# Performance work log

Measured on AMD Instinct MI355X. Metric: run time of the kernel, lower is better.

Reference implementation:

```python
import jax, jax.numpy as jnp
import numpy as np

N, E, B = 50000, 800000, 64
IN, H, OUT = 64, 128, 64


def _gcn_norm(edge_index, num_nodes):
    # PyG gcn_norm with add_self_loops=True: A_hat = A + I, norm = d^-1/2[src]*d^-1/2[dst]
    loop = jnp.arange(num_nodes)
    src = jnp.concatenate([edge_index[0], loop])
    dst = jnp.concatenate([edge_index[1], loop])
    deg = jax.ops.segment_sum(jnp.ones_like(dst, dtype=jnp.float32), dst,
                              num_segments=num_nodes)  # >= 1 due to self-loops
    dis = deg ** -0.5
    norm = dis[src] * dis[dst]  # [E+N]
    return src, dst, norm


def _gcn_layer(x, W, b, src, dst, norm, num_nodes):
    h = x @ W                                   # linear first (GCNConv order)
    msg = h[src] * norm[:, None]                # gather + normalize, [E+N, H]
    out = jax.ops.segment_sum(msg, dst, num_segments=num_nodes)  # scatter-add
    return out + b


def setup_inputs() -> dict:
    key = jax.random.key(0)
    ks = jax.random.split(key, 12)
    x = jax.random.normal(ks[0], (N, IN), dtype=jnp.float32)
    edge_index = jax.random.randint(ks[1], (2, E), 0, N, dtype=jnp.int64)
    batch = jnp.sort(jax.random.randint(ks[2], (N,), 0, B, dtype=jnp.int64))

    def lin(k, fan_in, fan_out):
        s = 1.0 / np.sqrt(fan_in)
        return jax.random.uniform(k, (fan_in, fan_out), jnp.float32, -s, s)

    return {
        "x": x, "edge_index": edge_index, "batch": batch,
        "W1": lin(ks[3], IN, H), "b1": jnp.zeros((H,), jnp.float32),
        "W2": lin(ks[4], H, H),  "b2": jnp.zeros((H,), jnp.float32),
        "W3": lin(ks[5], H, H),  "b3": jnp.zeros((H,), jnp.float32),
        "W4": lin(ks[6], H, OUT), "b4": jnp.zeros((OUT,), jnp.float32),
    }


def reference(x, edge_index, batch, W1, b1, W2, b2, W3, b3, W4, b4):
    src, dst, norm = _gcn_norm(edge_index, N)
    h = jax.nn.relu(_gcn_layer(x, W1, b1, src, dst, norm, N))
    h = jax.nn.relu(_gcn_layer(h, W2, b2, src, dst, norm, N))
    # global mean pool over graphs
    sums = jax.ops.segment_sum(h, batch, num_segments=B)          # [B, H]
    cnts = jax.ops.segment_sum(jnp.ones((N,), jnp.float32), batch, num_segments=B)
    pooled = sums / jnp.maximum(cnts, 1.0)[:, None]
    # MLP head
    return jax.nn.relu(pooled @ W3 + b3) @ W4 + b4                # [B, OUT]
```

## Files before the change

kernel.cpp:

```cpp
#include <hip/hip_runtime.h>


__device__ __forceinline__ float ldf(const void* p, long long i, int f32) {
    if (f32) return ((const float*)p)[i];
    unsigned int u = ((const unsigned short*)p)[i];
    return __uint_as_float(u << 16);
}
__device__ __forceinline__ float bfl(unsigned int u) { return __uint_as_float(u << 16); }
__device__ __forceinline__ float bfh(unsigned int u) { return __uint_as_float(u & 0xFFFF0000u); }
__device__ __forceinline__ int ld_idx(const int* p, long long i, int i64) {
    return i64 ? p[2 * i] : p[i];
}
__device__ __forceinline__ unsigned short f2bf(float v) {
    unsigned int x = __float_as_uint(v);
    return (unsigned short)((x + 0x7FFFu + ((x >> 16) & 1u)) >> 16);
}
__device__ __forceinline__ int clampi(int v, int lo, int hi) {
    return v < lo ? lo : (v > hi ? hi : v);
}

#define OW1 0
#define OB1 8192
#define OW2 8320
#define OB2 24704
// ... 69 lines not shown
        if (j < m) rank[base + j] = r[j];
}

__global__ void gnn_scan1(const int* __restrict__ cnt, int* __restrict__ excl,
                          int* __restrict__ sums, float* __restrict__ dis, int N) {
    __shared__ int sh[256];
    int t = threadIdx.x;
    int i = blockIdx.x * 256 + t;
    int v = (i < N) ? cnt[i] : 0;
    sh[t] = v;
    __syncthreads();
    for (int off = 1; off < 256; off <<= 1) {
        int a = (t >= off) ? sh[t - off] : 0;
        __syncthreads();
        sh[t] += a;
        __syncthreads();
    }
    if (i < N) {
        excl[i] = sh[t] - v;
        dis[i] = rsqrtf((float)v + 1.0f);
    }
    if (t == 255) sums[blockIdx.x] = sh[255];
}

__global__ void gnn_scan2(int* __restrict__ sums, int nb) {
    __shared__ int sh[256];
    int t = threadIdx.x;
    int v = (t < nb) ? sums[t] : 0;
    sh[t] = v;
    __syncthreads();
    for (int off = 1; off < 256; off <<= 1) {
        int a = (t >= off) ? sh[t - off] : 0;
        __syncthreads();
        sh[t] += a;
        __syncthreads();
    }
    if (t < nb) sums[t] = sh[t] - v;
}

template <bool SMALLN>
__global__ void gnn_fill(const int* __restrict__ ei, const int* __restrict__ excl,
                         const int* __restrict__ bsums, const int* __restrict__ rank,
                         void* __restrict__ csr, int E, int N,
                         const int* __restrict__ flags,
                         const void* __restrict__ x, const float* __restrict__ dis,
                         unsigned short* __restrict__ xb) {
    const int tid = blockIdx.x * 256 + threadIdx.x;
    const int i64 = flags[1];
    if (tid < E) {
        int s = clampi(ld_idx(ei, (long long)tid, i64), 0, N - 1);
        int d = clampi(ld_idx(ei, (long long)E + tid, i64), 0, N - 1);
        int pos = excl[d] + bsums[d >> 8] + rank[tid];
        if (SMALLN) ((unsigned short*)csr)[pos] = (unsigned short)s;
        else        ((int*)csr)[pos] = s;
    }
    const int f32 = flags[0];
    const int total = N * 16;
    const int stride = gridDim.x * 256;
    for (int j = tid; j < total; j += stride) {
        int n = j >> 4;
        float dn = dis[n];
        float v0, v1, v2, v3;
        if (f32) {
            float4 xv = ((const float4*)x)[j];
            v0 = xv.x; v1 = xv.y; v2 = xv.z; v3 = xv.w;
        } else {
            ushort4 xv = ((const ushort4*)x)[j];
            v0 = bfl(xv.x); v1 = bfl(xv.y); v2 = bfl(xv.z); v3 = bfl(xv.w);
        }
        ushort4 o;
        o.x = f2bf(v0 * dn); o.y = f2bf(v1 * dn);
        o.z = f2bf(v2 * dn); o.w = f2bf(v3 * dn);
        ((ushort4*)xb)[j] = o;
    }
}

template <bool SMALLN>
__device__ __forceinline__ int csr_at(const void* csr, int e) {
    return SMALLN ? (int)((const unsigned short*)csr)[e] : ((const int*)csr)[e];
}


template <bool SMALLN>
__global__ __launch_bounds__(128) void gnn_aggx_lin1(const unsigned short* __restrict__ xb,
                                                     const int* __restrict__ excl,
                                                     const int* __restrict__ bsums,
                                                     const void* __restrict__ csr,
                                                     const float* __restrict__ dis,
                                                     const float* __restrict__ Wf,
                                                     const float* __restrict__ bias,
                                                     int N, int E, float* __restrict__ out) {
    __shared__ float Xs[16 * 64];
    const int t = threadIdx.x;
    const int nbase = blockIdx.x * 16;
    const int wave = t >> 6;
    const int lane = t & 63;
    const int eslot = lane >> 3;
    const int fg = lane & 7;

    for (int pass = 0; pass < 8; ++pass) {
        const int ln = pass * 2 + wave;
        const int n = nbase + ln;
        float a0 = 0.f, a1 = 0.f, a2 = 0.f, a3 = 0.f;
        float a4 = 0.f, a5 = 0.f, a6 = 0.f, a7 = 0.f;
        if (n < N) {
            int beg = excl[n] + bsums[n >> 8];
            int end = (n + 1 < N) ? (excl[n + 1] + bsums[(n + 1) >> 8]) : E;
            for (int e = beg + eslot; e < end; e += 8) {
                int s = csr_at<SMALLN>(csr, e);
                uint4 u = *(const uint4*)(xb + (long long)s * 64 + fg * 8);
                a0 += bfl(u.x); a1 += bfh(u.x);
                a2 += bfl(u.y); a3 += bfh(u.y);
                a4 += bfl(u.z); a5 += bfh(u.z);
                a6 += bfl(u.w); a7 += bfh(u.w);
            }
        }
#pragma unroll
        for (int m = 8; m <= 32; m <<= 1) {
            a0 += __shfl_xor(a0, m); a1 += __shfl_xor(a1, m);
            a2 += __shfl_xor(a2, m); a3 += __shfl_xor(a3, m);
            a4 += __shfl_xor(a4, m); a5 += __shfl_xor(a5, m);
            a6 += __shfl_xor(a6, m); a7 += __shfl_xor(a7, m);
        }
        if (n < N && eslot == 0) {
            float dn = dis[n];
            uint4 u = *(const uint4*)(xb + (long long)n * 64 + fg * 8);
            float4 o0, o1;
            o0.x = (a0 + bfl(u.x)) * dn; o0.y = (a1 + bfh(u.x)) * dn;
            o0.z = (a2 + bfl(u.y)) * dn; o0.w = (a3 + bfh(u.y)) * dn;
            o1.x = (a4 + bfl(u.z)) * dn; o1.y = (a5 + bfh(u.z)) * dn;
            o1.z = (a6 + bfl(u.w)) * dn; o1.w = (a7 + bfh(u.w)) * dn;
            *(float4*)&Xs[ln * 64 + fg * 8]     = o0;
            *(float4*)&Xs[ln * 64 + fg * 8 + 4] = o1;
        }
    }
    __syncthreads();

    const int fgB = t & 31, ng = t >> 5;
    const int f0 = fgB * 4, n0 = ng * 4;
    const float4* Xs4 = (const float4*)Xs;
    const float4* Wp  = (const float4*)Wf;
    float4 acc[4];
#pragma unroll
    for (int j = 0; j < 4; ++j) acc[j] = make_float4(0.f, 0.f, 0.f, 0.f);
#pragma unroll 4
    for (int k4 = 0; k4 < 16; ++k4) {
        const float4 wa = Wp[(4 * k4 + 0) * 32 + fgB];
        const float4 wb = Wp[(4 * k4 + 1) * 32 + fgB];
        const float4 wc = Wp[(4 * k4 + 2) * 32 + fgB];
        const float4 wd = Wp[(4 * k4 + 3) * 32 + fgB];
#pragma unroll
        for (int j = 0; j < 4; ++j) {
            const float4 xv = Xs4[(n0 + j) * 16 + k4];
            acc[j].x = fmaf(xv.x, wa.x, acc[j].x); acc[j].y = fmaf(xv.x, wa.y, acc[j].y);
            acc[j].z = fmaf(xv.x, wa.z, acc[j].z); acc[j].w = fmaf(xv.x, wa.w, acc[j].w);
            acc[j].x = fmaf(xv.y, wb.x, acc[j].x); acc[j].y = fmaf(xv.y, wb.y, acc[j].y);
            acc[j].z = fmaf(xv.y, wb.z, acc[j].z); acc[j].w = fmaf(xv.y, wb.w, acc[j].w);
            acc[j].x = fmaf(xv.z, wc.x, acc[j].x); acc[j].y = fmaf(xv.z, wc.y, acc[j].y);
            acc[j].z = fmaf(xv.z, wc.z, acc[j].z); acc[j].w = fmaf(xv.z, wc.w, acc[j].w);
            acc[j].x = fmaf(xv.w, wd.x, acc[j].x); acc[j].y = fmaf(xv.w, wd.y, acc[j].y);
            acc[j].z = fmaf(xv.w, wd.z, acc[j].z); acc[j].w = fmaf(xv.w, wd.w, acc[j].w);
        }
    }
    const float4 b = *(const float4*)&bias[f0];
#pragma unroll
    for (int j = 0; j < 4; ++j) {
        int n = nbase + n0 + j;
        if (n >= N) continue;
        float4 a = acc[j];
        a.x = fmaxf(a.x + b.x, 0.f);
        a.y = fmaxf(a.y + b.y, 0.f);
        a.z = fmaxf(a.z + b.z, 0.f);
        a.w = fmaxf(a.w + b.w, 0.f);
        *(float4*)(out + (long long)n * 128 + f0) = a;
    }
}


template <int K, bool RELU, bool OUTBF>
__global__ __launch_bounds__(128) void gnn_linear(const float* __restrict__ X,
                                                  const float* __restrict__ Wf,
                                                  const float* __restrict__ bias,
                                                  const float* __restrict__ dis,
                                                  int N, void* __restrict__ out) {
    __shared__ float Xs[16 * K];
    const int t = threadIdx.x;
    const int nbase = blockIdx.x * 16;

#pragma unroll
    for (int it = 0; it < K / 32; ++it) {
        int i4 = t + it * 128;
        int n = nbase + (i4 * 4) / K;
        float4 v = make_float4(0.f, 0.f, 0.f, 0.f);
        if (n < N) v = ((const float4*)X)[(long long)nbase * (K / 4) + i4];
        ((float4*)Xs)[i4] = v;
    }
    __syncthreads();

    const int fg = t & 31, ng = t >> 5;
    const int f0 = fg * 4, n0 = ng * 4;
    const float4* Xs4 = (const float4*)Xs;
    const float4* Wp  = (const float4*)Wf;
    float4 acc[4];
#pragma unroll
    for (int j = 0; j < 4; ++j) acc[j] = make_float4(0.f, 0.f, 0.f, 0.f);
#pragma unroll 4
    for (int k4 = 0; k4 < K / 4; ++k4) {
        const float4 wa = Wp[(4 * k4 + 0) * 32 + fg];
        const float4 wb = Wp[(4 * k4 + 1) * 32 + fg];
        const float4 wc = Wp[(4 * k4 + 2) * 32 + fg];
        const float4 wd = Wp[(4 * k4 + 3) * 32 + fg];
#pragma unroll
        for (int j = 0; j < 4; ++j) {
            const float4 xv = Xs4[(n0 + j) * (K / 4) + k4];
            acc[j].x = fmaf(xv.x, wa.x, acc[j].x); acc[j].y = fmaf(xv.x, wa.y, acc[j].y);
            acc[j].z = fmaf(xv.x, wa.z, acc[j].z); acc[j].w = fmaf(xv.x, wa.w, acc[j].w);
            acc[j].x = fmaf(xv.y, wb.x, acc[j].x); acc[j].y = fmaf(xv.y, wb.y, acc[j].y);
            acc[j].z = fmaf(xv.y, wb.z, acc[j].z); acc[j].w = fmaf(xv.y, wb.w, acc[j].w);
            acc[j].x = fmaf(xv.z, wc.x, acc[j].x); acc[j].y = fmaf(xv.z, wc.y, acc[j].y);
            acc[j].z = fmaf(xv.z, wc.z, acc[j].z); acc[j].w = fmaf(xv.z, wc.w, acc[j].w);
            acc[j].x = fmaf(xv.w, wd.x, acc[j].x); acc[j].y = fmaf(xv.w, wd.y, acc[j].y);
            acc[j].z = fmaf(xv.w, wd.z, acc[j].z); acc[j].w = fmaf(xv.w, wd.w, acc[j].w);
        }
    }
#pragma unroll
    for (int j = 0; j < 4; ++j) {
        int n = nbase + n0 + j;
        if (n >= N) continue;
        float4 a = acc[j];
        if (RELU) {
            const float4 b = *(const float4*)&bias[f0];
            a.x = fmaxf(a.x + b.x, 0.f);
            a.y = fmaxf(a.y + b.y, 0.f);
            a.z = fmaxf(a.z + b.z, 0.f);
            a.w = fmaxf(a.w + b.w, 0.f);
        }
        if (OUTBF) {
            const float dn = dis[n];
            a.x *= dn; a.y *= dn; a.z *= dn; a.w *= dn;
            uint2 u;
            u.x = (unsigned int)f2bf(a.x) | ((unsigned int)f2bf(a.y) << 16);
            u.y = (unsigned int)f2bf(a.z) | ((unsigned int)f2bf(a.w) << 16);
            *(uint2*)((unsigned short*)out + (long long)n * 128 + f0) = u;
        } else {
            *(float4*)((float*)out + (long long)n * 128 + f0) = a;
        }
    }
}


template <bool SMALLN>
__global__ __launch_bounds__(256) void gnn_agg_bf(const unsigned short* __restrict__ A2,
                                                  const int* __restrict__ excl,
                                                  const int* __restrict__ bsums,
                                                  const void* __restrict__ csr,
                                                  const float* __restrict__ dis,
                                                  const float* __restrict__ bias,
                                                  float* __restrict__ outC, int N, int E) {
    const int t = threadIdx.x;
    const int lane = t & 63;
    const int n = blockIdx.x * 4 + (t >> 6);
    if (n >= N) return;
    const int eslot = lane >> 4;
    const int fg = lane & 15;
    float a0 = 0.f, a1 = 0.f, a2 = 0.f, a3 = 0.f;
    float a4 = 0.f, a5 = 0.f, a6 = 0.f, a7 = 0.f;
    int beg = excl[n] + bsums[n >> 8];
    int end = (n + 1 < N) ? (excl[n + 1] + bsums[(n + 1) >> 8]) : E;
    for (int e = beg + eslot; e < end; e += 4) {
        int s = csr_at<SMALLN>(csr, e);
        uint4 u = *(const uint4*)(A2 + (long long)s * 128 + fg * 8);
        a0 += bfl(u.x); a1 += bfh(u.x);
        a2 += bfl(u.y); a3 += bfh(u.y);
        a4 += bfl(u.z); a5 += bfh(u.z);
        a6 += bfl(u.w); a7 += bfh(u.w);
    }
#pragma unroll
    for (int m = 16; m <= 32; m <<= 1) {
        a0 += __shfl_xor(a0, m); a1 += __shfl_xor(a1, m);
        a2 += __shfl_xor(a2, m); a3 += __shfl_xor(a3, m);
        a4 += __shfl_xor(a4, m); a5 += __shfl_xor(a5, m);
        a6 += __shfl_xor(a6, m); a7 += __shfl_xor(a7, m);
    }
    if (lane < 16) {
        float dn = dis[n];
        uint4 u = *(const uint4*)(A2 + (long long)n * 128 + fg * 8);
        const float4 bA = *(const float4*)&bias[fg * 8];
        const float4 bB = *(const float4*)&bias[fg * 8 + 4];
        float4 o0, o1;
        o0.x = fmaxf((a0 + bfl(u.x)) * dn + bA.x, 0.f);
        o0.y = fmaxf((a1 + bfh(u.x)) * dn + bA.y, 0.f);
        o0.z = fmaxf((a2 + bfl(u.y)) * dn + bA.z, 0.f);
        o0.w = fmaxf((a3 + bfh(u.y)) * dn + bA.w, 0.f);
        o1.x = fmaxf((a4 + bfl(u.z)) * dn + bB.x, 0.f);
        o1.y = fmaxf((a5 + bfh(u.z)) * dn + bB.y, 0.f);
        o1.z = fmaxf((a6 + bfl(u.w)) * dn + bB.z, 0.f);
        o1.w = fmaxf((a7 + bfh(u.w)) * dn + bB.w, 0.f);
        *(float4*)(outC + (long long)n * 128 + fg * 8)     = o0;
        *(float4*)(outC + (long long)n * 128 + fg * 8 + 4) = o1;
    }
}


#define PSTRIP 32
__global__ __launch_bounds__(128) void gnn_pool(const float* __restrict__ h,
                                                const int* __restrict__ batch,
                                                const int* __restrict__ flags,
                                                float* __restrict__ pooled, int N, int B) {
    int i64 = flags[1];
    int f = threadIdx.x;
    int n0 = blockIdx.x * PSTRIP;
    if (n0 >= N) return;
    int nend = min(n0 + PSTRIP, N);
    int cur = clampi(ld_idx(batch, n0, i64), 0, B - 1);
    float acc = 0.0f;
    for (int n = n0; n < nend; ++n) {
        int b = clampi(ld_idx(batch, n, i64), 0, B - 1);
        if (b != cur) {
            atomicAdd(&pooled[cur * 128 + f], acc);
            acc = 0.0f; cur = b;
        }
        acc += h[(long long)n * 128 + f];
    }
    atomicAdd(&pooled[cur * 128 + f], acc);
}


__global__ __launch_bounds__(128) void gnn_head(const float* __restrict__ pooled,
                                                const int* __restrict__ batch,
                                                const float* __restrict__ W3,
                                                const float* __restrict__ b3,
                                                const float* __restrict__ W4,
                                                const float* __restrict__ b4,
                                                const int* __restrict__ flags,
                                                void* __restrict__ outv, int N) {
    __shared__ float xs[128];
    __shared__ float rs[128];
    __shared__ float cinv;
    int b = blockIdx.x, f = threadIdx.x;
    if (f == 0) {
        int i64 = flags[1];
        int L = 0, R = N;
        while (L < R) { int m = (L + R) >> 1; if (ld_idx(batch, m, i64) < b) L = m + 1; else R = m; }
        int lo = L;
        L = 0; R = N;
        while (L < R) { int m = (L + R) >> 1; if (ld_idx(batch, m, i64) < b + 1) L = m + 1; else R = m; }
        cinv = 1.0f / fmaxf((float)(L - lo), 1.0f);
    }
    __syncthreads();
    xs[f] = pooled[b * 128 + f] * cinv;
    __syncthreads();
    float acc = b3[f];
    for (int k = 0; k < 128; ++k) acc = fmaf(xs[k], W3[k * 128 + f], acc);
    rs[f] = fmaxf(acc, 0.f);
    __syncthreads();
    if (f < 64) {
        float a2 = b4[f];
        for (int k = 0; k < 128; ++k) a2 = fmaf(rs[k], W4[k * 64 + f], a2);
        if (flags[0]) ((float*)outv)[b * 64 + f] = a2;
        else          ((unsigned short*)outv)[b * 64 + f] = f2bf(a2);
    }
}


extern "C" void kernel_launch(void* const* d_in, const int* in_sizes, int n_in,
                              void* d_out, int out_size, void* d_ws, size_t ws_size,
                              hipStream_t stream) {
    const void* x  = d_in[0];
    const int* ei  = (const int*)d_in[1];
    const int* bat = (const int*)d_in[2];

    const int N = in_sizes[0] / 64;
    const int E = in_sizes[1] / 2;
    const int B = out_size / 64;
    const bool smalln = (N < 65536);

    char* p = (char*)d_ws;
    auto alloc = [&](size_t bytes) { void* q = (void*)p; p += (bytes + 255) & ~(size_t)255; return q; };
    int*   flags    = (int*)alloc(256);
    float* wsW      = (float*)alloc((size_t)OTOT * 4);
    int*   degcnt   = (int*)alloc((size_t)N * 4);
    float* dis      = (float*)alloc((size_t)N * 4);
    int*   excl     = (int*)alloc((size_t)N * 4);
    int*   bsums    = (int*)alloc(1024);
    int*   rank     = (int*)alloc((size_t)E * 4);
    void*  csr      = alloc((size_t)E * (smalln ? 2 : 4));
    unsigned short* xb = (unsigned short*)alloc((size_t)N * 64 * 2);
    float* H1       = (float*)alloc((size_t)N * 128 * 4);
    float* C2       = (float*)alloc((size_t)N * 128 * 4);
    unsigned short* A2 = (unsigned short*)alloc((size_t)N * 128 * 2);
    float* pooled   = (float*)alloc((size_t)B * 128 * 4);
    (void)ws_size; (void)n_in;

    const int nbN = (N + 255) / 256;

    gnn_prep<<<512, 256, 0, stream>>>(d_in[3], d_in[4], d_in[5], d_in[6],
                                      d_in[7], d_in[8], d_in[9], d_in[10],
                                      ei, flags, degcnt, pooled, wsW, N, B);

    gnn_hist<<<(E + 1023) / 1024, 256, 0, stream>>>(ei, E, N, flags, degcnt, rank);
    gnn_scan1<<<nbN, 256, 0, stream>>>(degcnt, excl, bsums, dis, N);
    gnn_scan2<<<1, 256, 0, stream>>>(bsums, nbN);
    if (smalln)
        gnn_fill<true><<<(E + 255) / 256, 256, 0, stream>>>(ei, excl, bsums, rank, csr, E, N,
                                                            flags, x, dis, xb);
    else
        gnn_fill<false><<<(E + 255) / 256, 256, 0, stream>>>(ei, excl, bsums, rank, csr, E, N,
                                                             flags, x, dis, xb);

    const int nlin = (N + 15) / 16;
    const int nagg = (N + 3) / 4;

    if (smalln)
        gnn_aggx_lin1<true><<<nlin, 128, 0, stream>>>(xb, excl, bsums, csr, dis,
                                                      wsW + OW1, wsW + OB1, N, E, H1);
    else
        gnn_aggx_lin1<false><<<nlin, 128, 0, stream>>>(xb, excl, bsums, csr, dis,
                                                       wsW + OW1, wsW + OB1, N, E, H1);

    gnn_linear<128, false, true><<<nlin, 128, 0, stream>>>(H1, wsW + OW2, wsW + OB2, dis, N, (void*)A2);
    if (smalln)
        gnn_agg_bf<true><<<nagg, 256, 0, stream>>>(A2, excl, bsums, csr, dis, wsW + OB2, C2, N, E);
    else
        gnn_agg_bf<false><<<nagg, 256, 0, stream>>>(A2, excl, bsums, csr, dis, wsW + OB2, C2, N, E);

    gnn_pool<<<(N + PSTRIP - 1) / PSTRIP, 128, 0, stream>>>(C2, bat, flags, pooled, N, B);
    gnn_head<<<B, 128, 0, stream>>>(pooled, bat, wsW + OW3, wsW + OB3,
                                    wsW + OW4, wsW + OB4, flags, d_out, N);
}
```

Measured before the change: 278.6 us.

## Fuse layer-1 aggregation, lin1 and lin2; remap aggregation to one node per lane group

Merges the layer-1 aggregate+linear kernel with the following 128x128 linear, so H1 stays in shared memory and its fp32 round trip through global memory plus one launch go away. Both aggregation kernels now give each lane group a whole node with a 4-way unrolled edge loop, replacing the edge-split layout and its cross-lane shuffle reduction, and the Xs tile row stride is padded to avoid bank conflicts. The cost is that each lane group processes a whole node serially, so load balance now depends on the degree variance within a wave.

Result: faster. 261.7 us (-6.1%).

```diff
diff --git a/kernel.cpp b/kernel.cpp
--- a/kernel.cpp
+++ b/kernel.cpp
@@ -175,168 +175,140 @@
 
 
 template <bool SMALLN>
-__global__ __launch_bounds__(128) void gnn_aggx_lin1(const unsigned short* __restrict__ xb,
-                                                     const int* __restrict__ excl,
-                                                     const int* __restrict__ bsums,
-                                                     const void* __restrict__ csr,
-                                                     const float* __restrict__ dis,
-                                                     const float* __restrict__ Wf,
-                                                     const float* __restrict__ bias,
-                                                     int N, int E, float* __restrict__ out) {
-    __shared__ float Xs[16 * 64];
+__global__ __launch_bounds__(128) void gnn_l1l2(const unsigned short* __restrict__ xb,
+                                                const int* __restrict__ excl,
+                                                const int* __restrict__ bsums,
+                                                const void* __restrict__ csr,
+                                                const float* __restrict__ dis,
+                                                const float* __restrict__ W1,
+                                                const float* __restrict__ b1,
+                                                const float* __restrict__ W2,
+                                                int N, int E,
+                                                unsigned short* __restrict__ A2) {
+    __shared__ float Xs[16 * 68];
+    __shared__ float Hs[16 * 128];
     const int t = threadIdx.x;
     const int nbase = blockIdx.x * 16;
-    const int wave = t >> 6;
     const int lane = t & 63;
-    const int eslot = lane >> 3;
+    const int nd = (t >> 6) * 8 + (lane >> 3);
     const int fg = lane & 7;
-
-    for (int pass = 0; pass < 8; ++pass) {
-        const int ln = pass * 2 + wave;
-        const int n = nbase + ln;
-        float a0 = 0.f, a1 = 0.f, a2 = 0.f, a3 = 0.f;
-        float a4 = 0.f, a5 = 0.f, a6 = 0.f, a7 = 0.f;
-        if (n < N) {
-            int beg = excl[n] + bsums[n >> 8];
-            int end = (n + 1 < N) ? (excl[n + 1] + bsums[(n + 1) >> 8]) : E;
-            for (int e = beg + eslot; e < end; e += 8) {
-                int s = csr_at<SMALLN>(csr, e);
-                uint4 u = *(const uint4*)(xb + (long long)s * 64 + fg * 8);
-                a0 += bfl(u.x); a1 += bfh(u.x);
-                a2 += bfl(u.y); a3 += bfh(u.y);
-                a4 += bfl(u.z); a5 += bfh(u.z);
-                a6 += bfl(u.w); a7 += bfh(u.w);
-            }
-        }
-#pragma unroll
-        for (int m = 8; m <= 32; m <<= 1) {
-            a0 += __shfl_xor(a0, m); a1 += __shfl_xor(a1, m);
-            a2 += __shfl_xor(a2, m); a3 += __shfl_xor(a3, m);
-            a4 += __shfl_xor(a4, m); a5 += __shfl_xor(a5, m);
-            a6 += __shfl_xor(a6, m); a7 += __shfl_xor(a7, m);
-        }
-        if (n < N && eslot == 0) {
-            float dn = dis[n];
-            uint4 u = *(const uint4*)(xb + (long long)n * 64 + fg * 8);
-            float4 o0, o1;
-            o0.x = (a0 + bfl(u.x)) * dn; o0.y = (a1 + bfh(u.x)) * dn;
-            o0.z = (a2 + bfl(u.y)) * dn; o0.w = (a3 + bfh(u.y)) * dn;
-            o1.x = (a4 + bfl(u.z)) * dn; o1.y = (a5 + bfh(u.z)) * dn;
-            o1.z = (a6 + bfl(u.w)) * dn; o1.w = (a7 + bfh(u.w)) * dn;
-            *(float4*)&Xs[ln * 64 + fg * 8]     = o0;
-            *(float4*)&Xs[ln * 64 + fg * 8 + 4] = o1;
-        }
+    const int n = nbase + nd;
+
+    if (n < N) {
+        const float dn = dis[n];
+        uint4 us = *(const uint4*)(xb + (long long)n * 64 + fg * 8);
+        float a0 = bfl(us.x), a1 = bfh(us.x), a2 = bfl(us.y), a3 = bfh(us.y);
+        float a4 = bfl(us.z), a5 = bfh(us.z), a6 = bfl(us.w), a7 = bfh(us.w);
+        int beg = excl[n] + bsums[n >> 8];
+        int end = (n + 1 < N) ? (excl[n + 1] + bsums[(n + 1) >> 8]) : E;
+        int e = beg;
+        for (; e + 4 <= end; e += 4) {
+            int s0 = csr_at<SMALLN>(csr, e),     s1 = csr_at<SMALLN>(csr, e + 1);
+            int s2 = csr_at<SMALLN>(csr, e + 2), s3 = csr_at<SMALLN>(csr, e + 3);
+            uint4 u0 = *(const uint4*)(xb + (long long)s0 * 64 + fg * 8);
+            uint4 u1 = *(const uint4*)(xb + (long long)s1 * 64 + fg * 8);
+            uint4 u2 = *(const uint4*)(xb + (long long)s2 * 64 + fg * 8);
+            uint4 u3 = *(const uint4*)(xb + (long long)s3 * 64 + fg * 8);
+            a0 += bfl(u0.x); a1 += bfh(u0.x); a2 += bfl(u0.y); a3 += bfh(u0.y);
+            a4 += bfl(u0.z); a5 += bfh(u0.z); a6 += bfl(u0.w); a7 += bfh(u0.w);
+            a0 += bfl(u1.x); a1 += bfh(u1.x); a2 += bfl(u1.y); a3 += bfh(u1.y);
+            a4 += bfl(u1.z); a5 += bfh(u1.z); a6 += bfl(u1.w); a7 += bfh(u1.w);
+            a0 += bfl(u2.x); a1 += bfh(u2.x); a2 += bfl(u2.y); a3 += bfh(u2.y);
+            a4 += bfl(u2.z); a5 += bfh(u2.z); a6 += bfl(u2.w); a7 += bfh(u2.w);
+            a0 += bfl(u3.x); a1 += bfh(u3.x); a2 += bfl(u3.y); a3 += bfh(u3.y);
+            a4 += bfl(u3.z); a5 += bfh(u3.z); a6 += bfl(u3.w); a7 += bfh(u3.w);
+        }
+        for (; e < end; ++e) {
+            int s = csr_at<SMALLN>(csr, e);
+            uint4 u = *(const uint4*)(xb + (long long)s * 64 + fg * 8);
+            a0 += bfl(u.x); a1 += bfh(u.x); a2 += bfl(u.y); a3 += bfh(u.y);
+            a4 += bfl(u.z); a5 += bfh(u.z); a6 += bfl(u.w); a7 += bfh(u.w);
+        }
+        float4 o0, o1;
+        o0.x = a0 * dn; o0.y = a1 * dn; o0.z = a2 * dn; o0.w = a3 * dn;
+        o1.x = a4 * dn; o1.y = a5 * dn; o1.z = a6 * dn; o1.w = a7 * dn;
+        *(float4*)&Xs[nd * 68 + fg * 8]     = o0;
+        *(float4*)&Xs[nd * 68 + fg * 8 + 4] = o1;
+    } else {
+        float4 z = make_float4(0.f, 0.f, 0.f, 0.f);
+        *(float4*)&Xs[nd * 68 + fg * 8]     = z;
+        *(float4*)&Xs[nd * 68 + fg * 8 + 4] = z;
     }
     __syncthreads();
 
     const int fgB = t & 31, ng = t >> 5;
     const int f0 = fgB * 4, n0 = ng * 4;
-    const float4* Xs4 = (const float4*)Xs;
-    const float4* Wp  = (const float4*)Wf;
-    float4 acc[4];
-#pragma unroll
-    for (int j = 0; j < 4; ++j) acc[j] = make_float4(0.f, 0.f, 0.f, 0.f);
+    {
+        const float4* Wp = (const float4*)W1;
+        float4 acc[4];
+#pragma unroll
+        for (int j = 0; j < 4; ++j) acc[j] = make_float4(0.f, 0.f, 0.f, 0.f);
 #pragma unroll 4
-    for (int k4 = 0; k4 < 16; ++k4) {
-        const float4 wa = Wp[(4 * k4 + 0) * 32 + fgB];
-        const float4 wb = Wp[(4 * k4 + 1) * 32 + fgB];
-        const float4 wc = Wp[(4 * k4 + 2) * 32 + fgB];
-        const float4 wd = Wp[(4 * k4 + 3) * 32 + fgB];
+        for (int k4 = 0; k4 < 16; ++k4) {
+            const float4 wa = Wp[(4 * k4 + 0) * 32 + fgB];
+            const float4 wb = Wp[(4 * k4 + 1) * 32 + fgB];
+            const float4 wc = Wp[(4 * k4 + 2) * 32 + fgB];
+            const float4 wd = Wp[(4 * k4 + 3) * 32 + fgB];
+#pragma unroll
+            for (int j = 0; j < 4; ++j) {
+                const float4 xv = *(const float4*)&Xs[(n0 + j) * 68 + k4 * 4];
+                acc[j].x = fmaf(xv.x, wa.x, acc[j].x); acc[j].y = fmaf(xv.x, wa.y, acc[j].y);
+                acc[j].z = fmaf(xv.x, wa.z, acc[j].z); acc[j].w = fmaf(xv.x, wa.w, acc[j].w);
+                acc[j].x = fmaf(xv.y, wb.x, acc[j].x); acc[j].y = fmaf(xv.y, wb.y, acc[j].y);
+                acc[j].z = fmaf(xv.y, wb.z, acc[j].z); acc[j].w = fmaf(xv.y, wb.w, acc[j].w);
+                acc[j].x = fmaf(xv.z, wc.x, acc[j].x); acc[j].y = fmaf(xv.z, wc.y, acc[j].y);
+                acc[j].z = fmaf(xv.z, wc.z, acc[j].z); acc[j].w = fmaf(xv.z, wc.w, acc[j].w);
+                acc[j].x = fmaf(xv.w, wd.x, acc[j].x); acc[j].y = fmaf(xv.w, wd.y, acc[j].y);
+                acc[j].z = fmaf(xv.w, wd.z, acc[j].z); acc[j].w = fmaf(xv.w, wd.w, acc[j].w);
+            }
+        }
+        const float4 b = *(const float4*)&b1[f0];
 #pragma unroll
         for (int j = 0; j < 4; ++j) {
-            const float4 xv = Xs4[(n0 + j) * 16 + k4];
-            acc[j].x = fmaf(xv.x, wa.x, acc[j].x); acc[j].y = fmaf(xv.x, wa.y, acc[j].y);
-            acc[j].z = fmaf(xv.x, wa.z, acc[j].z); acc[j].w = fmaf(xv.x, wa.w, acc[j].w);
-            acc[j].x = fmaf(xv.y, wb.x, acc[j].x); acc[j].y = fmaf(xv.y, wb.y, acc[j].y);
-            acc[j].z = fmaf(xv.y, wb.z, acc[j].z); acc[j].w = fmaf(xv.y, wb.w, acc[j].w);
-            acc[j].x = fmaf(xv.z, wc.x, acc[j].x); acc[j].y = fmaf(xv.z, wc.y, acc[j].y);
-            acc[j].z = fmaf(xv.z, wc.z, acc[j].z); acc[j].w = fmaf(xv.z, wc.w, acc[j].w);
-            acc[j].x = fmaf(xv.w, wd.x, acc[j].x); acc[j].y = fmaf(xv.w, wd.y, acc[j].y);
-            acc[j].z = fmaf(xv.w, wd.z, acc[j].z); acc[j].w = fmaf(xv.w, wd.w, acc[j].w);
-        }
-    }
-    const float4 b = *(const float4*)&bias[f0];
-#pragma unroll
-    for (int j = 0; j < 4; ++j) {
-        int n = nbase + n0 + j;
-        if (n >= N) continue;
-        float4 a = acc[j];
-        a.x = fmaxf(a.x + b.x, 0.f);
-        a.y = fmaxf(a.y + b.y, 0.f);
-        a.z = fmaxf(a.z + b.z, 0.f);
-        a.w = fmaxf(a.w + b.w, 0.f);
-        *(float4*)(out + (long long)n * 128 + f0) = a;
-    }
-}
-
-
-template <int K, bool RELU, bool OUTBF>
-__global__ __launch_bounds__(128) void gnn_linear(const float* __restrict__ X,
-                                                  const float* __restrict__ Wf,
-                                                  const float* __restrict__ bias,
-                                                  const float* __restrict__ dis,
-                                                  int N, void* __restrict__ out) {
-    __shared__ float Xs[16 * K];
-    const int t = threadIdx.x;
-    const int nbase = blockIdx.x * 16;
-
-#pragma unroll
-    for (int it = 0; it < K / 32; ++it) {
-        int i4 = t + it * 128;
-        int n = nbase + (i4 * 4) / K;
-        float4 v = make_float4(0.f, 0.f, 0.f, 0.f);
-        if (n < N) v = ((const float4*)X)[(long long)nbase * (K / 4) + i4];
-        ((float4*)Xs)[i4] = v;
-    }
-    __syncthreads();
-
-    const int fg = t & 31, ng = t >> 5;
-    const int f0 = fg * 4, n0 = ng * 4;
-    const float4* Xs4 = (const float4*)Xs;
-    const float4* Wp  = (const float4*)Wf;
-    float4 acc[4];
-#pragma unroll
-    for (int j = 0; j < 4; ++j) acc[j] = make_float4(0.f, 0.f, 0.f, 0.f);
-#pragma unroll 4
-    for (int k4 = 0; k4 < K / 4; ++k4) {
-        const float4 wa = Wp[(4 * k4 + 0) * 32 + fg];
-        const float4 wb = Wp[(4 * k4 + 1) * 32 + fg];
-        const float4 wc = Wp[(4 * k4 + 2) * 32 + fg];
-        const float4 wd = Wp[(4 * k4 + 3) * 32 + fg];
-#pragma unroll
-        for (int j = 0; j < 4; ++j) {
-            const float4 xv = Xs4[(n0 + j) * (K / 4) + k4];
-            acc[j].x = fmaf(xv.x, wa.x, acc[j].x); acc[j].y = fmaf(xv.x, wa.y, acc[j].y);
-            acc[j].z = fmaf(xv.x, wa.z, acc[j].z); acc[j].w = fmaf(xv.x, wa.w, acc[j].w);
-            acc[j].x = fmaf(xv.y, wb.x, acc[j].x); acc[j].y = fmaf(xv.y, wb.y, acc[j].y);
-            acc[j].z = fmaf(xv.y, wb.z, acc[j].z); acc[j].w = fmaf(xv.y, wb.w, acc[j].w);
-            acc[j].x = fmaf(xv.z, wc.x, acc[j].x); acc[j].y = fmaf(xv.z, wc.y, acc[j].y);
-            acc[j].z = fmaf(xv.z, wc.z, acc[j].z); acc[j].w = fmaf(xv.z, wc.w, acc[j].w);
-            acc[j].x = fmaf(xv.w, wd.x, acc[j].x); acc[j].y = fmaf(xv.w, wd.y, acc[j].y);
-            acc[j].z = fmaf(xv.w, wd.z, acc[j].z); acc[j].w = fmaf(xv.w, wd.w, acc[j].w);
-        }
-    }
-#pragma unroll
-    for (int j = 0; j < 4; ++j) {
-        int n = nbase + n0 + j;
-        if (n >= N) continue;
-        float4 a = acc[j];
-        if (RELU) {
-            const float4 b = *(const float4*)&bias[f0];
+            float4 a = acc[j];
             a.x = fmaxf(a.x + b.x, 0.f);
             a.y = fmaxf(a.y + b.y, 0.f);
             a.z = fmaxf(a.z + b.z, 0.f);
             a.w = fmaxf(a.w + b.w, 0.f);
-        }
-        if (OUTBF) {
-            const float dn = dis[n];
+            *(float4*)&Hs[(n0 + j) * 128 + f0] = a;
+        }
+    }
+    __syncthreads();
+    {
+        const float4* Wp = (const float4*)W2;
+        float4 acc[4];
+#pragma unroll
+        for (int j = 0; j < 4; ++j) acc[j] = make_float4(0.f, 0.f, 0.f, 0.f);
+#pragma unroll 4
+        for (int k4 = 0; k4 < 32; ++k4) {
+            const float4 wa = Wp[(4 * k4 + 0) * 32 + fgB];
+            const float4 wb = Wp[(4 * k4 + 1) * 32 + fgB];
+            const float4 wc = Wp[(4 * k4 + 2) * 32 + fgB];
+            const float4 wd = Wp[(4 * k4 + 3) * 32 + fgB];
+#pragma unroll
+            for (int j = 0; j < 4; ++j) {
+                const float4 xv = *(const float4*)&Hs[(n0 + j) * 128 + k4 * 4];
+                acc[j].x = fmaf(xv.x, wa.x, acc[j].x); acc[j].y = fmaf(xv.x, wa.y, acc[j].y);
+                acc[j].z = fmaf(xv.x, wa.z, acc[j].z); acc[j].w = fmaf(xv.x, wa.w, acc[j].w);
+                acc[j].x = fmaf(xv.y, wb.x, acc[j].x); acc[j].y = fmaf(xv.y, wb.y, acc[j].y);
+                acc[j].z = fmaf(xv.y, wb.z, acc[j].z); acc[j].w = fmaf(xv.y, wb.w, acc[j].w);
+                acc[j].x = fmaf(xv.z, wc.x, acc[j].x); acc[j].y = fmaf(xv.z, wc.y, acc[j].y);
+                acc[j].z = fmaf(xv.z, wc.z, acc[j].z); acc[j].w = fmaf(xv.z, wc.w, acc[j].w);
+                acc[j].x = fmaf(xv.w, wd.x, acc[j].x); acc[j].y = fmaf(xv.w, wd.y, acc[j].y);
+                acc[j].z = fmaf(xv.w, wd.z, acc[j].z); acc[j].w = fmaf(xv.w, wd.w, acc[j].w);
+            }
+        }
+#pragma unroll
+        for (int j = 0; j < 4; ++j) {
+            int nn = nbase + n0 + j;
+            if (nn >= N) continue;
+            const float dn = dis[nn];
+            float4 a = acc[j];
             a.x *= dn; a.y *= dn; a.z *= dn; a.w *= dn;
             uint2 u;
             u.x = (unsigned int)f2bf(a.x) | ((unsigned int)f2bf(a.y) << 16);
             u.y = (unsigned int)f2bf(a.z) | ((unsigned int)f2bf(a.w) << 16);
-            *(uint2*)((unsigned short*)out + (long long)n * 128 + f0) = u;
-        } else {
-            *(float4*)((float*)out + (long long)n * 128 + f0) = a;
+            *(uint2*)(A2 + (long long)nn * 128 + f0) = u;
         }
     }
 }
@@ -352,46 +324,51 @@
                                                   float* __restrict__ outC, int N, int E) {
     const int t = threadIdx.x;
     const int lane = t & 63;
-    const int n = blockIdx.x * 4 + (t >> 6);
+    const int n = blockIdx.x * 16 + (t >> 6) * 4 + (lane >> 4);
     if (n >= N) return;
-    const int eslot = lane >> 4;
     const int fg = lane & 15;
-    float a0 = 0.f, a1 = 0.f, a2 = 0.f, a3 = 0.f;
-    float a4 = 0.f, a5 = 0.f, a6 = 0.f, a7 = 0.f;
+    const float dn = dis[n];
+    uint4 us = *(const uint4*)(A2 + (long long)n * 128 + fg * 8);
+    float a0 = bfl(us.x), a1 = bfh(us.x), a2 = bfl(us.y), a3 = bfh(us.y);
+    float a4 = bfl(us.z), a5 = bfh(us.z), a6 = bfl(us.w), a7 = bfh(us.w);
     int beg = excl[n] + bsums[n >> 8];
     int end = (n + 1 < N) ? (excl[n + 1] + bsums[(n + 1) >> 8]) : E;
-    for (int e = beg + eslot; e < end; e += 4) {
+    int e = beg;
+    for (; e + 4 <= end; e += 4) {
+        int s0 = csr_at<SMALLN>(csr, e),     s1 = csr_at<SMALLN>(csr, e + 1);
+        int s2 = csr_at<SMALLN>(csr, e + 2), s3 = csr_at<SMALLN>(csr, e + 3);
+        uint4 u0 = *(const uint4*)(A2 + (long long)s0 * 128 + fg * 8);
+        uint4 u1 = *(const uint4*)(A2 + (long long)s1 * 128 + fg * 8);
+        uint4 u2 = *(const uint4*)(A2 + (long long)s2 * 128 + fg * 8);
+        uint4 u3 = *(const uint4*)(A2 + (long long)s3 * 128 + fg * 8);
+        a0 += bfl(u0.x); a1 += bfh(u0.x); a2 += bfl(u0.y); a3 += bfh(u0.y);
+        a4 += bfl(u0.z); a5 += bfh(u0.z); a6 += bfl(u0.w); a7 += bfh(u0.w);
+        a0 += bfl(u1.x); a1 += bfh(u1.x); a2 += bfl(u1.y); a3 += bfh(u1.y);
+        a4 += bfl(u1.z); a5 += bfh(u1.z); a6 += bfl(u1.w); a7 += bfh(u1.w);
+        a0 += bfl(u2.x); a1 += bfh(u2.x); a2 += bfl(u2.y); a3 += bfh(u2.y);
+        a4 += bfl(u2.z); a5 += bfh(u2.z); a6 += bfl(u2.w); a7 += bfh(u2.w);
+        a0 += bfl(u3.x); a1 += bfh(u3.x); a2 += bfl(u3.y); a3 += bfh(u3.y);
+        a4 += bfl(u3.z); a5 += bfh(u3.z); a6 += bfl(u3.w); a7 += bfh(u3.w);
+    }
+    for (; e < end; ++e) {
         int s = csr_at<SMALLN>(csr, e);
         uint4 u = *(const uint4*)(A2 + (long long)s * 128 + fg * 8);
-        a0 += bfl(u.x); a1 += bfh(u.x);
-        a2 += bfl(u.y); a3 += bfh(u.y);
-        a4 += bfl(u.z); a5 += bfh(u.z);
-        a6 += bfl(u.w); a7 += bfh(u.w);
-    }
-#pragma unroll
-    for (int m = 16; m <= 32; m <<= 1) {
-        a0 += __shfl_xor(a0, m); a1 += __shfl_xor(a1, m);
-        a2 += __shfl_xor(a2, m); a3 += __shfl_xor(a3, m);
-        a4 += __shfl_xor(a4, m); a5 += __shfl_xor(a5, m);
-        a6 += __shfl_xor(a6, m); a7 += __shfl_xor(a7, m);
-    }
-    if (lane < 16) {
-        float dn = dis[n];
-        uint4 u = *(const uint4*)(A2 + (long long)n * 128 + fg * 8);
-        const float4 bA = *(const float4*)&bias[fg * 8];
-        const float4 bB = *(const float4*)&bias[fg * 8 + 4];
-        float4 o0, o1;
-        o0.x = fmaxf((a0 + bfl(u.x)) * dn + bA.x, 0.f);
-        o0.y = fmaxf((a1 + bfh(u.x)) * dn + bA.y, 0.f);
-        o0.z = fmaxf((a2 + bfl(u.y)) * dn + bA.z, 0.f);
-        o0.w = fmaxf((a3 + bfh(u.y)) * dn + bA.w, 0.f);
-        o1.x = fmaxf((a4 + bfl(u.z)) * dn + bB.x, 0.f);
-        o1.y = fmaxf((a5 + bfh(u.z)) * dn + bB.y, 0.f);
-        o1.z = fmaxf((a6 + bfl(u.w)) * dn + bB.z, 0.f);
-        o1.w = fmaxf((a7 + bfh(u.w)) * dn + bB.w, 0.f);
-        *(float4*)(outC + (long long)n * 128 + fg * 8)     = o0;
-        *(float4*)(outC + (long long)n * 128 + fg * 8 + 4) = o1;
-    }
+        a0 += bfl(u.x); a1 += bfh(u.x); a2 += bfl(u.y); a3 += bfh(u.y);
+        a4 += bfl(u.z); a5 += bfh(u.z); a6 += bfl(u.w); a7 += bfh(u.w);
+    }
+    const float4 bA = *(const float4*)&bias[fg * 8];
+    const float4 bB = *(const float4*)&bias[fg * 8 + 4];
+    float4 o0, o1;
+    o0.x = fmaxf(a0 * dn + bA.x, 0.f);
+    o0.y = fmaxf(a1 * dn + bA.y, 0.f);
+    o0.z = fmaxf(a2 * dn + bA.z, 0.f);
+    o0.w = fmaxf(a3 * dn + bA.w, 0.f);
+    o1.x = fmaxf(a4 * dn + bB.x, 0.f);
+    o1.y = fmaxf(a5 * dn + bB.y, 0.f);
+    o1.z = fmaxf(a6 * dn + bB.z, 0.f);
+    o1.w = fmaxf(a7 * dn + bB.w, 0.f);
+    *(float4*)(outC + (long long)n * 128 + fg * 8)     = o0;
+    *(float4*)(outC + (long long)n * 128 + fg * 8 + 4) = o1;
 }
 
 
@@ -479,7 +456,6 @@
     int*   rank     = (int*)alloc((size_t)E * 4);
     void*  csr      = alloc((size_t)E * (smalln ? 2 : 4));
     unsigned short* xb = (unsigned short*)alloc((size_t)N * 64 * 2);
-    float* H1       = (float*)alloc((size_t)N * 128 * 4);
     float* C2       = (float*)alloc((size_t)N * 128 * 4);
     unsigned short* A2 = (unsigned short*)alloc((size_t)N * 128 * 2);
     float* pooled   = (float*)alloc((size_t)B * 128 * 4);
@@ -501,21 +477,19 @@
         gnn_fill<false><<<(E + 255) / 256, 256, 0, stream>>>(ei, excl, bsums, rank, csr, E, N,
                                                              flags, x, dis, xb);
 
-    const int nlin = (N + 15) / 16;
-    const int nagg = (N + 3) / 4;
+    const int nblk = (N + 15) / 16;
 
     if (smalln)
-        gnn_aggx_lin1<true><<<nlin, 128, 0, stream>>>(xb, excl, bsums, csr, dis,
-                                                      wsW + OW1, wsW + OB1, N, E, H1);
+        gnn_l1l2<true><<<nblk, 128, 0, stream>>>(xb, excl, bsums, csr, dis,
+                                                 wsW + OW1, wsW + OB1, wsW + OW2, N, E, A2);
     else
-        gnn_aggx_lin1<false><<<nlin, 128, 0, stream>>>(xb, excl, bsums, csr, dis,
-                                                       wsW + OW1, wsW + OB1, N, E, H1);
-
-    gnn_linear<128, false, true><<<nlin, 128, 0, stream>>>(H1, wsW + OW2, wsW + OB2, dis, N, (void*)A2);
+        gnn_l1l2<false><<<nblk, 128, 0, stream>>>(xb, excl, bsums, csr, dis,
+                                                  wsW + OW1, wsW + OB1, wsW + OW2, N, E, A2);
+
     if (smalln)
-        gnn_agg_bf<true><<<nagg, 256, 0, stream>>>(A2, excl, bsums, csr, dis, wsW + OB2, C2, N, E);
+        gnn_agg_bf<true><<<nblk, 256, 0, stream>>>(A2, excl, bsums, csr, dis, wsW + OB2, C2, N, E);
     else
-        gnn_agg_bf<false><<<nagg, 256, 0, stream>>>(A2, excl, bsums, csr, dis, wsW + OB2, C2, N, E);
+        gnn_agg_bf<false><<<nblk, 256, 0, stream>>>(A2, excl, bsums, csr, dis, wsW + OB2, C2, N, E);
 
     gnn_pool<<<(N + PSTRIP - 1) / PSTRIP, 128, 0, stream>>>(C2, bat, flags, pooled, N, B);
     gnn_head<<<B, 128, 0, stream>>>(pooled, bat, wsW + OW3, wsW + OB3,
```

## Aggregate before layer-2 linear and fuse linear2 with mean-pool

Applied to the files above, without the earlier changes.

Layer 2 now aggregates first (A_hat·H1) and then applies W2, instead of applying W2 first. Layer 1 writes its ReLU output, pre-scaled by deg^-1/2, directly as bf16. This removes the fp32 H1 round trip and the separate layer-2 linear kernel. The layer-2 linear, bias and ReLU are fused with the global pooling through segmented atomics, which removes the C2 buffer and the separate pool kernel. In exchange, the aggregation still writes an fp32 intermediate G, and pooling now does more atomic adds per block.

Result: slower. 312.8 us (+12.3%).

```diff
diff --git a/kernel.cpp b/kernel.cpp
--- a/kernel.cpp
+++ b/kernel.cpp
@@ -175,14 +175,15 @@
 
 
 template <bool SMALLN>
-__global__ __launch_bounds__(128) void gnn_aggx_lin1(const unsigned short* __restrict__ xb,
-                                                     const int* __restrict__ excl,
-                                                     const int* __restrict__ bsums,
-                                                     const void* __restrict__ csr,
-                                                     const float* __restrict__ dis,
-                                                     const float* __restrict__ Wf,
-                                                     const float* __restrict__ bias,
-                                                     int N, int E, float* __restrict__ out) {
+__global__ __launch_bounds__(128) void gnn_l1(const unsigned short* __restrict__ xb,
+                                              const int* __restrict__ excl,
+                                              const int* __restrict__ bsums,
+                                              const void* __restrict__ csr,
+                                              const float* __restrict__ dis,
+                                              const float* __restrict__ W1,
+                                              const float* __restrict__ b1,
+                                              int N, int E,
+                                              unsigned short* __restrict__ H1b) {
     __shared__ float Xs[16 * 64];
     const int t = threadIdx.x;
     const int nbase = blockIdx.x * 16;
@@ -225,6 +226,10 @@
             o1.z = (a6 + bfl(u.w)) * dn; o1.w = (a7 + bfh(u.w)) * dn;
             *(float4*)&Xs[ln * 64 + fg * 8]     = o0;
             *(float4*)&Xs[ln * 64 + fg * 8 + 4] = o1;
+        } else if (n >= N && eslot == 0) {
+            float4 z = make_float4(0.f, 0.f, 0.f, 0.f);
+            *(float4*)&Xs[ln * 64 + fg * 8]     = z;
+            *(float4*)&Xs[ln * 64 + fg * 8 + 4] = z;
         }
     }
     __syncthreads();
@@ -232,7 +237,7 @@
     const int fgB = t & 31, ng = t >> 5;
     const int f0 = fgB * 4, n0 = ng * 4;
     const float4* Xs4 = (const float4*)Xs;
-    const float4* Wp  = (const float4*)Wf;
+    const float4* Wp  = (const float4*)W1;
     float4 acc[4];
 #pragma unroll
     for (int j = 0; j < 4; ++j) acc[j] = make_float4(0.f, 0.f, 0.f, 0.f);
@@ -255,37 +260,91 @@
             acc[j].z = fmaf(xv.w, wd.z, acc[j].z); acc[j].w = fmaf(xv.w, wd.w, acc[j].w);
         }
     }
-    const float4 b = *(const float4*)&bias[f0];
+    const float4 b = *(const float4*)&b1[f0];
 #pragma unroll
     for (int j = 0; j < 4; ++j) {
         int n = nbase + n0 + j;
         if (n >= N) continue;
+        const float dn = dis[n];
         float4 a = acc[j];
-        a.x = fmaxf(a.x + b.x, 0.f);
-        a.y = fmaxf(a.y + b.y, 0.f);
-        a.z = fmaxf(a.z + b.z, 0.f);
-        a.w = fmaxf(a.w + b.w, 0.f);
-        *(float4*)(out + (long long)n * 128 + f0) = a;
-    }
-}
-
-
-template <int K, bool RELU, bool OUTBF>
-__global__ __launch_bounds__(128) void gnn_linear(const float* __restrict__ X,
-                                                  const float* __restrict__ Wf,
-                                                  const float* __restrict__ bias,
+        a.x = fmaxf(a.x + b.x, 0.f) * dn;
+        a.y = fmaxf(a.y + b.y, 0.f) * dn;
+        a.z = fmaxf(a.z + b.z, 0.f) * dn;
+        a.w = fmaxf(a.w + b.w, 0.f) * dn;
+        uint2 u;
+        u.x = (unsigned int)f2bf(a.x) | ((unsigned int)f2bf(a.y) << 16);
+        u.y = (unsigned int)f2bf(a.z) | ((unsigned int)f2bf(a.w) << 16);
+        *(uint2*)(H1b + (long long)n * 128 + f0) = u;
+    }
+}
+
+
+template <bool SMALLN>
+__global__ __launch_bounds__(256) void gnn_agg_bf(const unsigned short* __restrict__ H1b,
+                                                  const int* __restrict__ excl,
+                                                  const int* __restrict__ bsums,
+                                                  const void* __restrict__ csr,
                                                   const float* __restrict__ dis,
-                                                  int N, void* __restrict__ out) {
-    __shared__ float Xs[16 * K];
+                                                  float* __restrict__ G, int N, int E) {
+    const int t = threadIdx.x;
+    const int lane = t & 63;
+    const int n = blockIdx.x * 4 + (t >> 6);
+    if (n >= N) return;
+    const int eslot = lane >> 4;
+    const int fg = lane & 15;
+    float a0 = 0.f, a1 = 0.f, a2 = 0.f, a3 = 0.f;
+    float a4 = 0.f, a5 = 0.f, a6 = 0.f, a7 = 0.f;
+    if (eslot == 3) {
+        uint4 us = *(const uint4*)(H1b + (long long)n * 128 + fg * 8);
+        a0 = bfl(us.x); a1 = bfh(us.x); a2 = bfl(us.y); a3 = bfh(us.y);
+        a4 = bfl(us.z); a5 = bfh(us.z); a6 = bfl(us.w); a7 = bfh(us.w);
+    }
+    int beg = excl[n] + bsums[n >> 8];
+    int end = (n + 1 < N) ? (excl[n + 1] + bsums[(n + 1) >> 8]) : E;
+    for (int e = beg + eslot; e < end; e += 4) {
+        int s = csr_at<SMALLN>(csr, e);
+        uint4 u = *(const uint4*)(H1b + (long long)s * 128 + fg * 8);
+        a0 += bfl(u.x); a1 += bfh(u.x);
+        a2 += bfl(u.y); a3 += bfh(u.y);
+        a4 += bfl(u.z); a5 += bfh(u.z);
+        a6 += bfl(u.w); a7 += bfh(u.w);
+    }
+#pragma unroll
+    for (int m = 16; m <= 32; m <<= 1) {
+        a0 += __shfl_xor(a0, m); a1 += __shfl_xor(a1, m);
+        a2 += __shfl_xor(a2, m); a3 += __shfl_xor(a3, m);
+        a4 += __shfl_xor(a4, m); a5 += __shfl_xor(a5, m);
+        a6 += __shfl_xor(a6, m); a7 += __shfl_xor(a7, m);
+    }
+    if (eslot == 0) {
+        const float dn = dis[n];
+        float4 o0, o1;
+        o0.x = a0 * dn; o0.y = a1 * dn; o0.z = a2 * dn; o0.w = a3 * dn;
+        o1.x = a4 * dn; o1.y = a5 * dn; o1.z = a6 * dn; o1.w = a7 * dn;
+        *(float4*)(G + (long long)n * 128 + fg * 8)     = o0;
+        *(float4*)(G + (long long)n * 128 + fg * 8 + 4) = o1;
+    }
+}
+
+
+__global__ __launch_bounds__(128) void gnn_lin2pool(const float* __restrict__ X,
+                                                    const float* __restrict__ Wf,
+                                                    const float* __restrict__ bias,
+                                                    const int* __restrict__ batch,
+                                                    const int* __restrict__ flags,
+                                                    float* __restrict__ pooled,
+                                                    int N, int B) {
+    __shared__ float Xs[16 * 128];
     const int t = threadIdx.x;
     const int nbase = blockIdx.x * 16;
-
-#pragma unroll
-    for (int it = 0; it < K / 32; ++it) {
+    const int i64 = flags[1];
+
+#pragma unroll
+    for (int it = 0; it < 4; ++it) {
         int i4 = t + it * 128;
-        int n = nbase + (i4 * 4) / K;
+        int n = nbase + (i4 * 4) / 128;
         float4 v = make_float4(0.f, 0.f, 0.f, 0.f);
-        if (n < N) v = ((const float4*)X)[(long long)nbase * (K / 4) + i4];
+        if (n < N) v = ((const float4*)X)[(long long)nbase * 32 + i4];
         ((float4*)Xs)[i4] = v;
     }
     __syncthreads();
@@ -298,14 +357,14 @@
 #pragma unroll
     for (int j = 0; j < 4; ++j) acc[j] = make_float4(0.f, 0.f, 0.f, 0.f);
 #pragma unroll 4
-    for (int k4 = 0; k4 < K / 4; ++k4) {
+    for (int k4 = 0; k4 < 32; ++k4) {
         const float4 wa = Wp[(4 * k4 + 0) * 32 + fg];
         const float4 wb = Wp[(4 * k4 + 1) * 32 + fg];
         const float4 wc = Wp[(4 * k4 + 2) * 32 + fg];
         const float4 wd = Wp[(4 * k4 + 3) * 32 + fg];
 #pragma unroll
         for (int j = 0; j < 4; ++j) {
-            const float4 xv = Xs4[(n0 + j) * (K / 4) + k4];
+            const float4 xv = Xs4[(n0 + j) * 32 + k4];
             acc[j].x = fmaf(xv.x, wa.x, acc[j].x); acc[j].y = fmaf(xv.x, wa.y, acc[j].y);
             acc[j].z = fmaf(xv.x, wa.z, acc[j].z); acc[j].w = fmaf(xv.x, wa.w, acc[j].w);
             acc[j].x = fmaf(xv.y, wb.x, acc[j].x); acc[j].y = fmaf(xv.y, wb.y, acc[j].y);
@@ -316,106 +375,35 @@
             acc[j].z = fmaf(xv.w, wd.z, acc[j].z); acc[j].w = fmaf(xv.w, wd.w, acc[j].w);
         }
     }
+    const float4 b = *(const float4*)&bias[f0];
+    int bprev = -1;
+    float4 s = make_float4(0.f, 0.f, 0.f, 0.f);
 #pragma unroll
     for (int j = 0; j < 4; ++j) {
         int n = nbase + n0 + j;
-        if (n >= N) continue;
+        if (n >= N) break;
         float4 a = acc[j];
-        if (RELU) {
-            const float4 b = *(const float4*)&bias[f0];
-            a.x = fmaxf(a.x + b.x, 0.f);
-            a.y = fmaxf(a.y + b.y, 0.f);
-            a.z = fmaxf(a.z + b.z, 0.f);
-            a.w = fmaxf(a.w + b.w, 0.f);
-        }
-        if (OUTBF) {
-            const float dn = dis[n];
-            a.x *= dn; a.y *= dn; a.z *= dn; a.w *= dn;
-            uint2 u;
-            u.x = (unsigned int)f2bf(a.x) | ((unsigned int)f2bf(a.y) << 16);
-            u.y = (unsigned int)f2bf(a.z) | ((unsigned int)f2bf(a.w) << 16);
-            *(uint2*)((unsigned short*)out + (long long)n * 128 + f0) = u;
+        a.x = fmaxf(a.x + b.x, 0.f);
+        a.y = fmaxf(a.y + b.y, 0.f);
+        a.z = fmaxf(a.z + b.z, 0.f);
+        a.w = fmaxf(a.w + b.w, 0.f);
+        int bj = clampi(ld_idx(batch, n, i64), 0, B - 1);
+        if (bj != bprev) {
+            if (bprev >= 0) {
+                float* pp = &pooled[bprev * 128 + f0];
+                atomicAdd(pp + 0, s.x); atomicAdd(pp + 1, s.y);
+                atomicAdd(pp + 2, s.z); atomicAdd(pp + 3, s.w);
+            }
+            s = a; bprev = bj;
         } else {
-            *(float4*)((float*)out + (long long)n * 128 + f0) = a;
-        }
-    }
-}
-
-
-template <bool SMALLN>
-__global__ __launch_bounds__(256) void gnn_agg_bf(const unsigned short* __restrict__ A2,
-                                                  const int* __restrict__ excl,
-                                                  const int* __restrict__ bsums,
-                                                  const void* __restrict__ csr,
-                                                  const float* __restrict__ dis,
-                                                  const float* __restrict__ bias,
-                                                  float* __restrict__ outC, int N, int E) {
-    const int t = threadIdx.x;
-    const int lane = t & 63;
-    const int n = blockIdx.x * 4 + (t >> 6);
-    if (n >= N) return;
-    const int eslot = lane >> 4;
-    const int fg = lane & 15;
-    float a0 = 0.f, a1 = 0.f, a2 = 0.f, a3 = 0.f;
-    float a4 = 0.f, a5 = 0.f, a6 = 0.f, a7 = 0.f;
-    int beg = excl[n] + bsums[n >> 8];
-    int end = (n + 1 < N) ? (excl[n + 1] + bsums[(n + 1) >> 8]) : E;
-    for (int e = beg + eslot; e < end; e += 4) {
-        int s = csr_at<SMALLN>(csr, e);
-        uint4 u = *(const uint4*)(A2 + (long long)s * 128 + fg * 8);
-        a0 += bfl(u.x); a1 += bfh(u.x);
-        a2 += bfl(u.y); a3 += bfh(u.y);
-        a4 += bfl(u.z); a5 += bfh(u.z);
-        a6 += bfl(u.w); a7 += bfh(u.w);
-    }
-#pragma unroll
-    for (int m = 16; m <= 32; m <<= 1) {
-        a0 += __shfl_xor(a0, m); a1 += __shfl_xor(a1, m);
-        a2 += __shfl_xor(a2, m); a3 += __shfl_xor(a3, m);
-        a4 += __shfl_xor(a4, m); a5 += __shfl_xor(a5, m);
-        a6 += __shfl_xor(a6, m); a7 += __shfl_xor(a7, m);
-    }
-    if (lane < 16) {
-        float dn = dis[n];
-        uint4 u = *(const uint4*)(A2 + (long long)n * 128 + fg * 8);
-        const float4 bA = *(const float4*)&bias[fg * 8];
-        const float4 bB = *(const float4*)&bias[fg * 8 + 4];
-        float4 o0, o1;
-        o0.x = fmaxf((a0 + bfl(u.x)) * dn + bA.x, 0.f);
-        o0.y = fmaxf((a1 + bfh(u.x)) * dn + bA.y, 0.f);
-        o0.z = fmaxf((a2 + bfl(u.y)) * dn + bA.z, 0.f);
-        o0.w = fmaxf((a3 + bfh(u.y)) * dn + bA.w, 0.f);
-        o1.x = fmaxf((a4 + bfl(u.z)) * dn + bB.x, 0.f);
-        o1.y = fmaxf((a5 + bfh(u.z)) * dn + bB.y, 0.f);
-        o1.z = fmaxf((a6 + bfl(u.w)) * dn + bB.z, 0.f);
-        o1.w = fmaxf((a7 + bfh(u.w)) * dn + bB.w, 0.f);
-        *(float4*)(outC + (long long)n * 128 + fg * 8)     = o0;
-        *(float4*)(outC + (long long)n * 128 + fg * 8 + 4) = o1;
-    }
-}
-
-
-#define PSTRIP 32
-__global__ __launch_bounds__(128) void gnn_pool(const float* __restrict__ h,
-                                                const int* __restrict__ batch,
-                                                const int* __restrict__ flags,
-                                                float* __restrict__ pooled, int N, int B) {
-    int i64 = flags[1];
-    int f = threadIdx.x;
-    int n0 = blockIdx.x * PSTRIP;
-    if (n0 >= N) return;
-    int nend = min(n0 + PSTRIP, N);
-    int cur = clampi(ld_idx(batch, n0, i64), 0, B - 1);
-    float acc = 0.0f;
-    for (int n = n0; n < nend; ++n) {
-        int b = clampi(ld_idx(batch, n, i64), 0, B - 1);
-        if (b != cur) {
-            atomicAdd(&pooled[cur * 128 + f], acc);
-            acc = 0.0f; cur = b;
-        }
-        acc += h[(long long)n * 128 + f];
-    }
-    atomicAdd(&pooled[cur * 128 + f], acc);
+            s.x += a.x; s.y += a.y; s.z += a.z; s.w += a.w;
+        }
+    }
+    if (bprev >= 0) {
+        float* pp = &pooled[bprev * 128 + f0];
+        atomicAdd(pp + 0, s.x); atomicAdd(pp + 1, s.y);
+        atomicAdd(pp + 2, s.z); atomicAdd(pp + 3, s.w);
+    }
 }
 
 
@@ -478,10 +466,9 @@
     int*   bsums    = (int*)alloc(1024);
     int*   rank     = (int*)alloc((size_t)E * 4);
     void*  csr      = alloc((size_t)E * (smalln ? 2 : 4));
-    unsigned short* xb = (unsigned short*)alloc((size_t)N * 64 * 2);
-    float* H1       = (float*)alloc((size_t)N * 128 * 4);
-    float* C2       = (float*)alloc((size_t)N * 128 * 4);
-    unsigned short* A2 = (unsigned short*)alloc((size_t)N * 128 * 2);
+    unsigned short* xb  = (unsigned short*)alloc((size_t)N * 64 * 2);
+    unsigned short* H1b = (unsigned short*)alloc((size_t)N * 128 * 2);
+    float* G        = (float*)alloc((size_t)N * 128 * 4);
     float* pooled   = (float*)alloc((size_t)B * 128 * 4);
     (void)ws_size; (void)n_in;
 
@@ -501,23 +488,22 @@
         gnn_fill<false><<<(E + 255) / 256, 256, 0, stream>>>(ei, excl, bsums, rank, csr, E, N,
                                                              flags, x, dis, xb);
 
-    const int nlin = (N + 15) / 16;
-    const int nagg = (N + 3) / 4;
+    const int nblk = (N + 15) / 16;
 
     if (smalln)
-        gnn_aggx_lin1<true><<<nlin, 128, 0, stream>>>(xb, excl, bsums, csr, dis,
-                                                      wsW + OW1, wsW + OB1, N, E, H1);
+        gnn_l1<true><<<nblk, 128, 0, stream>>>(xb, excl, bsums, csr, dis,
+                                               wsW + OW1, wsW + OB1, N, E, H1b);
     else
-        gnn_aggx_lin1<false><<<nlin, 128, 0, stream>>>(xb, excl, bsums, csr, dis,
-                                                       wsW + OW1, wsW + OB1, N, E, H1);
-
-    gnn_linear<128, false, true><<<nlin, 128, 0, stream>>>(H1, wsW + OW2, wsW + OB2, dis, N, (void*)A2);
+        gnn_l1<false><<<nblk, 128, 0, stream>>>(xb, excl, bsums, csr, dis,
+                                                wsW + OW1, wsW + OB1, N, E, H1b);
+
     if (smalln)
-        gnn_agg_bf<true><<<nagg, 256, 0, stream>>>(A2, excl, bsums, csr, dis, wsW + OB2, C2, N, E);
+        gnn_agg_bf<true><<<(N + 3) / 4, 256, 0, stream>>>(H1b, excl, bsums, csr, dis, G, N, E);
     else
-        gnn_agg_bf<false><<<nagg, 256, 0, stream>>>(A2, excl, bsums, csr, dis, wsW + OB2, C2, N, E);
-
-    gnn_pool<<<(N + PSTRIP - 1) / PSTRIP, 128, 0, stream>>>(C2, bat, flags, pooled, N, B);
+        gnn_agg_bf<false><<<(N + 3) / 4, 256, 0, stream>>>(H1b, excl, bsums, csr, dis, G, N, E);
+
+    gnn_lin2pool<<<nblk, 128, 0, stream>>>(G, wsW + OW2, wsW + OB2, bat, flags, pooled, N, B);
+
     gnn_head<<<B, 128, 0, stream>>>(pooled, bat, wsW + OW3, wsW + OB3,
                                     wsW + OW4, wsW + OB4, flags, d_out, N);
 }
```
